# Kernel tuning notes

Hardware: AMD Instinct MI355X
Metric: run time of the kernel (lower is better)

Reference implementation:

```python
import jax, jax.numpy as jnp
import numpy as np

N = 100000   # nodes per batched graph
E = 1000000  # edges per batched graph
G = 64       # graphs in batch
D = 64       # node feature dim
H = 128      # hidden dim
L = 3        # num GCN layers
EPS = 1e-5


def setup_inputs() -> dict:
    key = jax.random.key(0)
    ks = jax.random.split(key, 20)
    def xavier(k, shape):
        fan_in, fan_out = shape[0], shape[1]
        lim = np.sqrt(6.0 / (fan_in + fan_out)).astype(np.float32)
        return jax.random.uniform(k, shape, jnp.float32, -lim, lim)
    return {
        'kernel_x': jax.random.normal(ks[0], (N, D), jnp.float32),
        'kernel_edge_index': jax.random.randint(ks[1], (2, E), 0, N, jnp.int32),
        'kernel_batch': jnp.sort(jax.random.randint(ks[2], (N,), 0, G, jnp.int32)),
        'design_x': jax.random.normal(ks[3], (N, D), jnp.float32),
        'design_edge_index': jax.random.randint(ks[4], (2, E), 0, N, jnp.int32),
        'design_batch': jnp.sort(jax.random.randint(ks[5], (N,), 0, G, jnp.int32)),
        'pragma_count': 4,
        'enc_W': xavier(ks[6], (D, H)), 'enc_b': jnp.zeros((H,), jnp.float32),
        'conv_W': jnp.stack([xavier(ks[7 + i], (H, H)) for i in range(L)]),
        'conv_b': jnp.zeros((L, H), jnp.float32),
        'ln_w': jnp.ones((L, H), jnp.float32), 'ln_b': jnp.zeros((L, H), jnp.float32),
        'head_W1': xavier(ks[10], (2 * H, H)), 'head_b1': jnp.zeros((H,), jnp.float32),
        'head_W2': xavier(ks[11], (H, H // 2)), 'head_b2': jnp.zeros((H // 2,), jnp.float32),
        'head_W3': xavier(ks[12], (H // 2, 1)), 'head_b3': jnp.zeros((1,), jnp.float32),
    }


def _gcn(x, W, b, src, dst):
    # PyG GCNConv: x' = D^{-1/2} (A + I) D^{-1/2} (x W) + b
    n = x.shape[0]
    xw = x @ W
    loop = jnp.arange(n, dtype=src.dtype)
    s = jnp.concatenate([src, loop])
    d = jnp.concatenate([dst, loop])
    deg = jax.ops.segment_sum(jnp.ones_like(d, dtype=x.dtype), d, num_segments=n)
    dinv = jax.lax.rsqrt(deg)  # deg >= 1 due to self-loops
    norm = dinv[s] * dinv[d]                       # [E+N]
    msgs = xw[s] * norm[:, None]                   # gather-transform
    return jax.ops.segment_sum(msgs, d, num_segments=n) + b


def _graph_layernorm(x, w, b, batch, num_graphs):
    # PyG LayerNorm mode='graph': normalize over all nodes+channels per graph
    n, c = x.shape
    cnt = jax.ops.segment_sum(jnp.ones((n,), x.dtype), batch, num_segments=num_graphs) * c
    mean = jax.ops.segment_sum(x.sum(axis=1), batch, num_segments=num_graphs) / cnt
    xc = x - mean[batch][:, None]
    var = jax.ops.segment_sum((xc * xc).sum(axis=1), batch, num_segments=num_graphs) / cnt
    out = xc * jax.lax.rsqrt(var + EPS)[batch][:, None]
    return out * w + b


def _encode_graph(x, edge_index, batch, enc_W, enc_b, conv_W, conv_b, ln_w, ln_b):
    src, dst = edge_index[0], edge_index[1]
    h = x @ enc_W + enc_b
    for i in range(L):
        h = _gcn(h, conv_W[i], conv_b[i], src, dst)
        h = _graph_layernorm(h, ln_w[i], ln_b[i], batch, G)
        if i < L - 1:
            h = jax.nn.relu(h)
    return jax.ops.segment_sum(h, batch, num_segments=G)  # global_add_pool -> [G, H]


def reference(kernel_x, kernel_edge_index, kernel_batch,
              design_x, design_edge_index, design_batch, pragma_count,
              enc_W, enc_b, conv_W, conv_b, ln_w, ln_b,
              head_W1, head_b1, head_W2, head_b2, head_W3, head_b3):
    design_repr = _encode_graph(design_x, design_edge_index, design_batch,
                                enc_W, enc_b, conv_W, conv_b, ln_w, ln_b)
    kernel_repr = _encode_graph(kernel_x, kernel_edge_index, kernel_batch,
                                enc_W, enc_b, conv_W, conv_b, ln_w, ln_b)
    combined = jnp.concatenate([kernel_repr, design_repr], axis=-1)  # [G, 2H]
    h = jax.nn.relu(combined @ head_W1 + head_b1)  # dropout is identity at eval
    h = jax.nn.relu(h @ head_W2 + head_b2)
    return h @ head_W3 + head_b3  # delta_pred [G, 1]
```

## Files before the change

### kernel.cpp

```cpp
#include <hip/hip_runtime.h>


#define TPB 256
#define FILL_CHUNK 2048

typedef __attribute__((ext_vector_type(8))) short bf16x8;
typedef __attribute__((ext_vector_type(8))) unsigned short u16x8;
typedef __attribute__((ext_vector_type(4))) float f32x4;
typedef __attribute__((ext_vector_type(2))) float f32x2;

__device__ __forceinline__ float bf2f(unsigned short s) {
  unsigned int u = ((unsigned int)s) << 16;
  float f;
  __builtin_memcpy(&f, &u, 4);
  return f;
}

__device__ __forceinline__ unsigned short f2bf(float f) {
  unsigned int u;
  __builtin_memcpy(&u, &f, 4);
  u = (u + 0x7FFF + ((u >> 16) & 1)) >> 16;
  return (unsigned short)u;
}

__device__ __forceinline__ void pk_acc(f32x2& acc, unsigned u) {
  union { unsigned q[2]; f32x2 f; } t;
  t.q[0] = u << 16;
  t.q[1] = u & 0xffff0000u;
  asm("v_pk_add_f32 %0, %0, %1" : "+v"(acc) : "v"(t.f));
}


__global__ __launch_bounds__(TPB) void count_dst_k(const int* __restrict__ kei,
                                                   const int* __restrict__ dei,
                                                   int* __restrict__ cnt, int E) {
  int e = blockIdx.x * TPB + threadIdx.x;
  if (e >= 2 * E) return;
  int d = (e < E) ? kei[E + e] : dei[e] + 100000;
  atomicAdd(&cnt[d], 1);
}

__global__ __launch_bounds__(TPB) void prep_node_k(const int* __restrict__ cnt,
                                                   float* __restrict__ dinv,
                                                   const int* __restrict__ kb,
                                                   const int* __restrict__ db,
                                                   int* __restrict__ batchU,
                                                   int* __restrict__ gstart,
                                                   int N, int NT) {
  int i = blockIdx.x * TPB + threadIdx.x;
  if (i >= NT) return;
  dinv[i] = 1.0f / sqrtf((float)cnt[i] + 1.0f);
  int b = (i < N) ? kb[i] : db[i - N] + 64;
  batchU[i] = b;
  if (i == 0) {
    for (int g = 0; g <= b; ++g) gstart[g] = 0;
  } else {
    int pb = (i - 1 < N) ? kb[i - 1] : db[i - 1 - N] + 64;
    for (int g = pb + 1; g <= b; ++g) gstart[g] = i;
  }
  if (i == NT - 1) {
    for (int g = b + 1; g <= 128; ++g) gstart[g] = NT;
  }
}


__global__ __launch_bounds__(TPB) void scan_partial_k(const int* __restrict__ cnt,
                                                      int* __restrict__ bsum, int n) {
  __shared__ int sd[TPB];
  int t = threadIdx.x, i0 = blockIdx.x * 512 + t * 2;
  int s = 0;
  if (i0 < n) s += cnt[i0];
  if (i0 + 1 < n) s += cnt[i0 + 1];
  sd[t] = s;
  __syncthreads();
  for (int st = TPB / 2; st > 0; st >>= 1) {
    if (t < st) sd[t] += sd[t + st];
    __syncthreads();
  }
  if (t == 0) bsum[blockIdx.x] = sd[0];
}

__global__ __launch_bounds__(512) void scan_small_k(const int* __restrict__ bsum,
                                                    int* __restrict__ bpre, int P,
                                                    int* __restrict__ rowptr, int n) {
  __shared__ int sd[512];
  int t = threadIdx.x;
  int v = (t < P) ? bsum[t] : 0;
  sd[t] = v;
  __syncthreads();
  for (int d = 1; d < 512; d <<= 1) {
    int w = (t >= d) ? sd[t - d] : 0;
    __syncthreads();
    sd[t] += w;
    __syncthreads();
  }
  if (t < P) bpre[t] = sd[t] - v;
  if (t == 511) rowptr[n] = sd[511];
}

__global__ __launch_bounds__(TPB) void scan_fill_k(const int* __restrict__ cnt,
                                                   const int* __restrict__ bpre,
                                                   int* __restrict__ rowptr,
                                                   int* __restrict__ cursor, int n) {
  __shared__ int sd[TPB];
  int t = threadIdx.x, i0 = blockIdx.x * 512 + t * 2;
  int c0 = (i0 < n) ? cnt[i0] : 0;
  int c1 = (i0 + 1 < n) ? cnt[i0 + 1] : 0;
  int s = c0 + c1;
  sd[t] = s;
  __syncthreads();
  for (int d = 1; d < TPB; d <<= 1) {
    int w = (t >= d) ? sd[t - d] : 0;
    __syncthreads();
    sd[t] += w;
    __syncthreads();
  }
  int ex = sd[t] - s + bpre[blockIdx.x];
  if (i0 < n) { rowptr[i0] = ex; cursor[i0] = ex; }
  if (i0 + 1 < n) { rowptr[i0 + 1] = ex + c0; cursor[i0 + 1] = ex + c0; }
}


__global__ __launch_bounds__(TPB) void csrfill_k(const int* __restrict__ kei,
                                                 const int* __restrict__ dei,
                                                 int* __restrict__ cursor,
                                                 int* __restrict__ csr_src,
                                                 int E, int NT) {
  int range = blockIdx.x & 7;
  int chunk = blockIdx.x >> 3;
  int nper = (NT + 7) >> 3;
  int lo = range * nper;
  int hi = lo + nper; if (hi > NT) hi = NT;
  int base = chunk * FILL_CHUNK;
  int end = base + FILL_CHUNK; if (end > 2 * E) end = 2 * E;
  const int N = NT >> 1;
  for (int e = base + threadIdx.x; e < end; e += TPB) {
    int s, d;
    if (e < E) { s = kei[e]; d = kei[E + e]; }
    else       { s = dei[e - E] + N; d = dei[e] + N; }
    if (d >= lo && d < hi) {
      int p = atomicAdd(&cursor[d], 1);
      csr_src[p] = s;
    }
  }
}


__global__ __launch_bounds__(TPB) void wprep_k(const float* __restrict__ encW,
                                               const float* __restrict__ convW,
                                               unsigned short* __restrict__ encWt,
                                               unsigned short* __restrict__ convWt) {
  int idx = blockIdx.x * TPB + threadIdx.x;
  if (idx < 64 * 128) {
    int k = idx >> 7, c = idx & 127;
    encWt[c * 64 + k] = f2bf(encW[idx]);
  }
  idx -= 64 * 128;
  if (idx >= 0 && idx < 3 * 128 * 128) {
    int l = idx >> 14, r = idx & 16383;
    int k = r >> 7, c = r & 127;
    convWt[l * 16384 + c * 128 + k] = f2bf(convW[idx]);
  }
}


template <int K, bool BIAS, bool LNRELU, bool SCALE, bool F32IN>
__global__ __launch_bounds__(TPB) void mfma_gemm_k(
    const unsigned short* __restrict__ A, const float* __restrict__ X1,
    const float* __restrict__ X2, int nsplit,
    const unsigned short* __restrict__ Wt,
    const float* __restrict__ bias, unsigned short* __restrict__ C, int nrows,
    const int* __restrict__ batch, const float* __restrict__ meanA,
    const float* __restrict__ rsigA, const float* __restrict__ lnw,
    const float* __restrict__ lnb, const float* __restrict__ dinv) {
  __shared__ short As[128 * K];
  __shared__ short Bs[128 * K];
  const int tid = threadIdx.x;
  const int r0 = blockIdx.x << 7;
  const int lane = tid & 63;
  const int wv = tid >> 6;
  const int lr = lane & 15, lg = lane >> 4;
  constexpr int CPR = K / 8;

  for (int i = tid; i < 128 * CPR; i += TPB) {
    int rloc = i / CPR, cb = i % CPR;
    int r = r0 + rloc;
    bf16x8 v = {0, 0, 0, 0, 0, 0, 0, 0};
    if (r < nrows) {
      if (F32IN) {
        const float* Af = (r < nsplit ? X1 + (long)r * K : X2 + (long)(r - nsplit) * K) + cb * 8;
        float4 f0 = *(const float4*)Af;
        float4 f1 = *(const float4*)(Af + 4);
        v[0] = (short)f2bf(f0.x); v[1] = (short)f2bf(f0.y);
        v[2] = (short)f2bf(f0.z); v[3] = (short)f2bf(f0.w);
        v[4] = (short)f2bf(f1.x); v[5] = (short)f2bf(f1.y);
        v[6] = (short)f2bf(f1.z); v[7] = (short)f2bf(f1.w);
      } else {
        v = *(const bf16x8*)(A + (long)r * K + cb * 8);
        if (LNRELU) {
          int g = batch[r];
          float m = meanA[g], rs = rsigA[g];
          int c0 = cb * 8;
#pragma unroll
          for (int j = 0; j < 8; ++j) {
            float f = bf2f((unsigned short)v[j]);
            f = (f - m) * rs * lnw[c0 + j] + lnb[c0 + j];
            f = fmaxf(f, 0.f);
            v[j] = (short)f2bf(f);
          }
        }
      }
    }
    int sb = cb ^ (rloc & 7);
    *(bf16x8*)(&As[rloc * K + sb * 8]) = v;
  }
  for (int i = tid; i < 128 * CPR; i += TPB) {
    int rloc = i / CPR, cb = i % CPR;
    bf16x8 v = *(const bf16x8*)(Wt + (long)rloc * K + cb * 8);
    int sb = cb ^ (rloc & 7);
    *(bf16x8*)(&Bs[rloc * K + sb * 8]) = v;
  }
  __syncthreads();

  f32x4 acc[2][8];
#pragma unroll
  for (int m = 0; m < 2; ++m)
#pragma unroll
    for (int n = 0; n < 8; ++n) acc[m][n] = {0.f, 0.f, 0.f, 0.f};

  const int wrow = wv * 32;
#pragma unroll
  for (int k0 = 0; k0 < K; k0 += 32) {
    const int cbk = (k0 >> 3) + lg;
    bf16x8 a[2], b[8];
#pragma unroll
    for (int m = 0; m < 2; ++m) {
      int rr = wrow + m * 16 + lr;
      int sb = cbk ^ (rr & 7);
      a[m] = *(const bf16x8*)(&As[rr * K + sb * 8]);
    }
#pragma unroll
    for (int n = 0; n < 8; ++n) {
      int rr = n * 16 + lr;
      int sb = cbk ^ (rr & 7);
      b[n] = *(const bf16x8*)(&Bs[rr * K + sb * 8]);
    }
#pragma unroll
    for (int m = 0; m < 2; ++m)
#pragma unroll
      for (int n = 0; n < 8; ++n)
        acc[m][n] = __builtin_amdgcn_mfma_f32_16x16x32_bf16(a[m], b[n], acc[m][n], 0, 0, 0);
  }

  float bv[8];
#pragma unroll
  for (int n = 0; n < 8; ++n) bv[n] = BIAS ? bias[n * 16 + lr] : 0.f;
#pragma unroll
  for (int m = 0; m < 2; ++m) {
#pragma unroll
    for (int ri = 0; ri < 4; ++ri) {
      int r = r0 + wrow + m * 16 + lg * 4 + ri;
      if (r < nrows) {
        float dv = SCALE ? dinv[r] : 1.f;
#pragma unroll
        for (int n = 0; n < 8; ++n) {
          float v = acc[m][n][ri] + bv[n];
          if (SCALE) v *= dv;
          C[(long)r * 128 + n * 16 + lr] = f2bf(v);
        }
      }
    }
  }
}


__global__ __launch_bounds__(TPB) void aggregate_k(
    const uint4* __restrict__ xws, const int* __restrict__ rowptr,
    const int* __restrict__ csr, const float* __restrict__ dinv,
    const float* __restrict__ bias, uint4* __restrict__ outb,
    float2* __restrict__ rs2, int n) {
  int wave = threadIdx.x >> 6, lane = threadIdx.x & 63;
  int d = (blockIdx.x << 2) + wave;
  if (d >= n) return;
  const int g3 = lane >> 4, cpos = lane & 15;
  f32x2 a01 = {0.f, 0.f}, a23 = {0.f, 0.f}, a45 = {0.f, 0.f}, a67 = {0.f, 0.f};

  int p0 = rowptr[d], p1 = rowptr[d + 1];
  for (int base = p0; base < p1; base += 64) {
    int idx = base + lane;
    int sl = (idx < p1) ? csr[idx] : 0;
    int cnt = p1 - base;
    if (cnt > 64) cnt = 64;
    for (int e = 0; e < cnt; e += 8) {
      int e0 = e + g3, e1 = e + 4 + g3;
      int s0 = __shfl(sl, e0);
      int s1 = __shfl(sl, e1);
      uint4 u0 = xws[(long)s0 * 16 + cpos];
      uint4 u1 = xws[(long)s1 * 16 + cpos];
      if (e0 < cnt) {
        pk_acc(a01, u0.x);
        pk_acc(a23, u0.y);
        pk_acc(a45, u0.z);
        pk_acc(a67, u0.w);
      }
      if (e1 < cnt) {
        pk_acc(a01, u1.x);
        pk_acc(a23, u1.y);
        pk_acc(a45, u1.z);
        pk_acc(a67, u1.w);
      }
    }
  }

  float acc[8] = {a01.x, a01.y, a23.x, a23.y, a45.x, a45.y, a67.x, a67.y};
#pragma unroll
  for (int j = 0; j < 8; ++j) {
    acc[j] += __shfl_xor(acc[j], 16);
    acc[j] += __shfl_xor(acc[j], 32);
  }

  uint4 su = xws[(long)d * 16 + cpos];
  float dd = dinv[d];
  float sv[8];
  sv[0] = __uint_as_float(su.x << 16);
  sv[1] = __uint_as_float(su.x & 0xffff0000u);
  sv[2] = __uint_as_float(su.y << 16);
  sv[3] = __uint_as_float(su.y & 0xffff0000u);
  sv[4] = __uint_as_float(su.z << 16);
  sv[5] = __uint_as_float(su.z & 0xffff0000u);
  sv[6] = __uint_as_float(su.w << 16);
  sv[7] = __uint_as_float(su.w & 0xffff0000u);
  const float4* b4 = (const float4*)bias;
  float4 bb0 = b4[cpos * 2];
  float4 bb1 = b4[cpos * 2 + 1];
  float val[8];
  val[0] = (acc[0] + sv[0]) * dd + bb0.x;
  val[1] = (acc[1] + sv[1]) * dd + bb0.y;
  val[2] = (acc[2] + sv[2]) * dd + bb0.z;
  val[3] = (acc[3] + sv[3]) * dd + bb0.w;
  val[4] = (acc[4] + sv[4]) * dd + bb1.x;
  val[5] = (acc[5] + sv[5]) * dd + bb1.y;
  val[6] = (acc[6] + sv[6]) * dd + bb1.z;
  val[7] = (acc[7] + sv[7]) * dd + bb1.w;

  if (g3 == 0) {
    uint4 o;
    o.x = (unsigned)f2bf(val[0]) | ((unsigned)f2bf(val[1]) << 16);
    o.y = (unsigned)f2bf(val[2]) | ((unsigned)f2bf(val[3]) << 16);
    o.z = (unsigned)f2bf(val[4]) | ((unsigned)f2bf(val[5]) << 16);
    o.w = (unsigned)f2bf(val[6]) | ((unsigned)f2bf(val[7]) << 16);
    outb[(long)d * 16 + cpos] = o;
  }

  float s1 = 0.f, s2 = 0.f;
#pragma unroll
  for (int j = 0; j < 8; ++j) {
    s1 += val[j];
    s2 += val[j] * val[j];
  }
#pragma unroll
  for (int m = 8; m >= 1; m >>= 1) {
    s1 += __shfl_xor(s1, m);
    s2 += __shfl_xor(s2, m);
  }
  if (lane == 0) rs2[d] = make_float2(s1, s2);
}


__global__ __launch_bounds__(TPB) void gstats_k(const float2* __restrict__ rs2,
                                                const int* __restrict__ gstart,
                                                float* __restrict__ meanA,
                                                float* __restrict__ rsigA,
                                                float* __restrict__ cntA) {
  __shared__ double sd1[TPB], sd2[TPB];
  int g = blockIdx.x, t = threadIdx.x;
  int n0 = gstart[g], n1 = gstart[g + 1];
  double s1 = 0, s2 = 0;
  for (int i = n0 + t; i < n1; i += TPB) {
    float2 v = rs2[i];
    s1 += v.x; s2 += v.y;
  }
  sd1[t] = s1; sd2[t] = s2;
  __syncthreads();
  for (int st = TPB / 2; st > 0; st >>= 1) {
    if (t < st) { sd1[t] += sd1[t + st]; sd2[t] += sd2[t + st]; }
    __syncthreads();
  }
  if (t == 0) {
    double cntd = (double)(n1 - n0) * 128.0;
    if (cntd > 0.0) {
      double mean = sd1[0] / cntd;
      double var = sd2[0] / cntd - mean * mean;
      if (var < 0.0) var = 0.0;
      meanA[g] = (float)mean;
      rsigA[g] = (float)(1.0 / sqrt(var + 1e-5));
    } else {
      meanA[g] = 0.f;
      rsigA[g] = 0.f;
    }
    cntA[g] = (float)(n1 - n0);
  }
}


__global__ __launch_bounds__(TPB) void pool_k(const unsigned short* __restrict__ x,
                                              const int* __restrict__ gstart,
                                              float* __restrict__ part) {
  __shared__ float red[16][132];
  int g = blockIdx.x >> 3, s = blockIdx.x & 7;
  int tid = threadIdx.x;
  int ro = tid >> 4, c8 = tid & 15;
  int n0 = gstart[g], n1 = gstart[g + 1];
  float acc[8];
#pragma unroll
  for (int j = 0; j < 8; ++j) acc[j] = 0.f;
  for (int nn = n0 + s + ro * 8; nn < n1; nn += 8 * 16) {
    u16x8 v = *(const u16x8*)(x + (long)nn * 128 + c8 * 8);
#pragma unroll
    for (int j = 0; j < 8; ++j) acc[j] += bf2f(v[j]);
  }
#pragma unroll
  for (int j = 0; j < 8; ++j) red[ro][c8 * 8 + j] = acc[j];
  __syncthreads();
  for (int st = 8; st > 0; st >>= 1) {
    if (ro < st) {
#pragma unroll
      for (int j = 0; j < 8; ++j) red[ro][c8 * 8 + j] += red[ro + st][c8 * 8 + j];
    }
    __syncthreads();
  }
  if (tid < 128) part[((long)s * 128 + g) * 128 + tid] = red[0][tid];
}


__global__ __launch_bounds__(TPB) void head_k(
    const float* __restrict__ part, const float* __restrict__ meanU,
    const float* __restrict__ rsigU, const float* __restrict__ cntU,
    const float* __restrict__ lnw2, const float* __restrict__ lnb2,
    const float* __restrict__ W1, const float* __restrict__ b1,
    const float* __restrict__ W2, const float* __restrict__ b2,
    const float* __restrict__ W3, const float* __restrict__ b3,
    float* __restrict__ out) {
  __shared__ float ps[256];
  __shared__ float prt[256];
  __shared__ float h1[128];
  __shared__ float h2[64];
  int g = blockIdx.x, tid = threadIdx.x;
  {
    int j = tid & 127, side = tid >> 7;
    int gg = side ? 64 + g : g;
    float S = 0.f;
#pragma unroll
    for (int s = 0; s < 8; ++s) S += part[((long)s * 128 + gg) * 128 + j];
    float m = meanU[gg], r = rsigU[gg], c = cntU[gg];
    ps[tid] = lnw2[j] * r * (S - m * c) + lnb2[j] * c;
  }
  __syncthreads();
  {
    int j = tid & 127, half = tid >> 7;
    float acc = 0.f;
    const float* w = W1 + (size_t)half * 128 * 128 + j;
    const float* p = ps + half * 128;
#pragma unroll 8
    for (int k = 0; k < 128; ++k) acc = fmaf(p[k], w[(size_t)k * 128], acc);
    prt[tid] = acc;
    __syncthreads();
    if (tid < 128) h1[tid] = fmaxf(prt[tid] + prt[tid + 128] + b1[tid], 0.f);
    __syncthreads();
  }
  {
    int j = tid & 63, q = tid >> 6;
    float acc = 0.f;
    const float* w = W2 + (size_t)q * 32 * 64 + j;
    const float* p = h1 + q * 32;
#pragma unroll 8
    for (int k = 0; k < 32; ++k) acc = fmaf(p[k], w[(size_t)k * 64], acc);
    prt[tid] = acc;
    __syncthreads();
    if (tid < 64)
      h2[tid] = fmaxf(prt[tid] + prt[tid + 64] + prt[tid + 128] + prt[tid + 192] + b2[tid], 0.f);
    __syncthreads();
  }
  if (tid < 64) {
    float v = h2[tid] * W3[tid];
#pragma unroll
    for (int m = 32; m >= 1; m >>= 1) v += __shfl_xor(v, m);
    if (tid == 0) out[g] = v + b3[0];
  }
}


extern "C" void kernel_launch(void* const* d_in, const int* in_sizes, int n_in,
                              void* d_out, int out_size, void* d_ws, size_t ws_size,
                              hipStream_t stream) {
  const int N = in_sizes[2];
  const int E = in_sizes[1] / 2;
  const int NT = 2 * N, ET = 2 * E;
  const int H = 128, L = 3;
  (void)n_in; (void)ws_size; (void)out_size;

  const float* kernel_x = (const float*)d_in[0];
  const int* kernel_ei  = (const int*)d_in[1];
  const int* kernel_b   = (const int*)d_in[2];
  const float* design_x = (const float*)d_in[3];
  const int* design_ei  = (const int*)d_in[4];
  const int* design_b   = (const int*)d_in[5];
  const float* encW  = (const float*)d_in[7];
  const float* encB  = (const float*)d_in[8];
  const float* convW = (const float*)d_in[9];
  const float* convB = (const float*)d_in[10];
  const float* lnw   = (const float*)d_in[11];
  const float* lnb   = (const float*)d_in[12];
  const float* W1 = (const float*)d_in[13];
  const float* b1 = (const float*)d_in[14];
  const float* W2 = (const float*)d_in[15];
  const float* b2 = (const float*)d_in[16];
  const float* W3 = (const float*)d_in[17];
  const float* b3 = (const float*)d_in[18];
  float* out = (float*)d_out;

  char* ws = (char*)d_ws;
  size_t off = 0;
  auto alloc = [&](size_t bytes) -> void* {
    void* p = ws + off;
    off = (off + bytes + 511) & ~(size_t)511;
    return p;
  };
  unsigned short* bufA = (unsigned short*)alloc((size_t)NT * H * 2);
  unsigned short* bufX = (unsigned short*)alloc((size_t)NT * H * 2);
  float* dinv    = (float*)alloc((size_t)NT * 4);
  int* cntI      = (int*)alloc((size_t)NT * 4);
  int* rowptr    = (int*)alloc((size_t)(NT + 1) * 4);
  int* cursor    = (int*)alloc((size_t)NT * 4);
  int* csr_src   = (int*)alloc((size_t)ET * 4);
  int* batchU    = (int*)alloc((size_t)NT * 4);
  int* gstart    = (int*)alloc((size_t)129 * 4);
  float2* rs2    = (float2*)alloc((size_t)NT * 8);
  float* meanS   = (float*)alloc((size_t)128 * 4);
  float* rsigS   = (float*)alloc((size_t)128 * 4);
  float* cntS    = (float*)alloc((size_t)128 * 4);
  float* meanU   = (float*)alloc((size_t)128 * 4);
  float* rsigU   = (float*)alloc((size_t)128 * 4);
  float* cntU    = (float*)alloc((size_t)128 * 4);
  float* part    = (float*)alloc((size_t)8 * 128 * 128 * 4);
  int* bsum      = (int*)alloc(512 * 4);
  int* bpre      = (int*)alloc(512 * 4);
  unsigned short* encWt  = (unsigned short*)alloc((size_t)128 * 64 * 2);
  unsigned short* convWt = (unsigned short*)alloc((size_t)L * 128 * 128 * 2);

  const int gNT   = (NT + TPB - 1) / TPB;
  const int gET   = (ET + TPB - 1) / TPB;
  const int gGemm = (NT + 127) / 128;
  const int gAgg  = (NT + 3) / 4;
  const int P     = (NT + 511) / 512;
  const int gFill = 8 * ((ET + FILL_CHUNK - 1) / FILL_CHUNK);

  wprep_k<<<(64 * 128 + 3 * 128 * 128 + TPB - 1) / TPB, TPB, 0, stream>>>(
      encW, convW, encWt, convWt);

  hipMemsetAsync(cntI, 0, (size_t)NT * 4, stream);
  count_dst_k<<<gET, TPB, 0, stream>>>(kernel_ei, design_ei, cntI, E);
  prep_node_k<<<gNT, TPB, 0, stream>>>(cntI, dinv, kernel_b, design_b, batchU,
                                       gstart, N, NT);
  scan_partial_k<<<P, TPB, 0, stream>>>(cntI, bsum, NT);
  scan_small_k<<<1, 512, 0, stream>>>(bsum, bpre, P, rowptr, NT);
  scan_fill_k<<<P, TPB, 0, stream>>>(cntI, bpre, rowptr, cursor, NT);
  csrfill_k<<<gFill, TPB, 0, stream>>>(kernel_ei, design_ei, cursor, csr_src, E, NT);

  mfma_gemm_k<64, true, false, false, true><<<gGemm, TPB, 0, stream>>>(
      nullptr, kernel_x, design_x, N, encWt, encB, bufA, NT,
      nullptr, nullptr, nullptr, nullptr, nullptr, nullptr);

  for (int i = 0; i < L; ++i) {
    float* mS = (i == L - 1) ? meanU : meanS;
    float* rS = (i == L - 1) ? rsigU : rsigS;
    float* cS = (i == L - 1) ? cntU : cntS;
    if (i == 0)
      mfma_gemm_k<128, false, false, true, false><<<gGemm, TPB, 0, stream>>>(
          bufA, nullptr, nullptr, 0, convWt + (size_t)i * H * H, nullptr, bufX, NT,
          nullptr, nullptr, nullptr, nullptr, nullptr, dinv);
    else
      mfma_gemm_k<128, false, true, true, false><<<gGemm, TPB, 0, stream>>>(
          bufA, nullptr, nullptr, 0, convWt + (size_t)i * H * H, nullptr, bufX, NT,
          batchU, meanS, rsigS, lnw + (size_t)(i - 1) * H,
          lnb + (size_t)(i - 1) * H, dinv);
    aggregate_k<<<gAgg, TPB, 0, stream>>>((const uint4*)bufX, rowptr, csr_src,
                                          dinv, convB + (size_t)i * H,
                                          (uint4*)bufA, rs2, NT);
    gstats_k<<<128, TPB, 0, stream>>>(rs2, gstart, mS, rS, cS);
  }
  pool_k<<<128 * 8, TPB, 0, stream>>>(bufA, gstart, part);

  head_k<<<64, TPB, 0, stream>>>(part, meanU, rsigU, cntU,
                                 lnw + (size_t)(L - 1) * H, lnb + (size_t)(L - 1) * H,
                                 W1, b1, W2, b2, W3, b3, out);
}
```

Baseline: 629.2 us.

## Range-partition degree counting, unroll aggregation gathers to four, enlarge fill chunk

The degree-count kernel now has each block scan a chunk of edges and apply atomics only for destinations in one of eight node ranges. This matches the range-partitioned CSR fill and is meant to improve atomic locality in L2. The aggregation loop now issues four independent gathers per iteration instead of two, raising memory-level parallelism. FILL_CHUNK doubles, which halves the grid for both the count and fill kernels. The trade-offs are that every edge index is read eight times during counting, and the wider unroll adds register pressure.

Result: no change. 625.4 us (-0.6%).

```diff
diff --git a/kernel.cpp b/kernel.cpp
--- a/kernel.cpp
+++ b/kernel.cpp
@@ -2,7 +2,7 @@
 
 
 #define TPB 256
-#define FILL_CHUNK 2048
+#define FILL_CHUNK 4096
 
 typedef __attribute__((ext_vector_type(8))) short bf16x8;
 typedef __attribute__((ext_vector_type(8))) unsigned short u16x8;
@@ -33,11 +33,20 @@
 
 __global__ __launch_bounds__(TPB) void count_dst_k(const int* __restrict__ kei,
                                                    const int* __restrict__ dei,
-                                                   int* __restrict__ cnt, int E) {
-  int e = blockIdx.x * TPB + threadIdx.x;
-  if (e >= 2 * E) return;
-  int d = (e < E) ? kei[E + e] : dei[e] + 100000;
-  atomicAdd(&cnt[d], 1);
+                                                   int* __restrict__ cnt,
+                                                   int E, int NT) {
+  int range = blockIdx.x & 7;
+  int chunk = blockIdx.x >> 3;
+  int nper = (NT + 7) >> 3;
+  int lo = range * nper;
+  int hi = lo + nper; if (hi > NT) hi = NT;
+  int base = chunk * FILL_CHUNK;
+  int end = base + FILL_CHUNK; if (end > 2 * E) end = 2 * E;
+  const int N = NT >> 1;
+  for (int e = base + threadIdx.x; e < end; e += TPB) {
+    int d = (e < E) ? kei[E + e] : dei[e] + N;
+    if (d >= lo && d < hi) atomicAdd(&cnt[d], 1);
+  }
 }
 
 __global__ __launch_bounds__(TPB) void prep_node_k(const int* __restrict__ cnt,
@@ -285,32 +294,37 @@
   const int g3 = lane >> 4, cpos = lane & 15;
   f32x2 a01 = {0.f, 0.f}, a23 = {0.f, 0.f}, a45 = {0.f, 0.f}, a67 = {0.f, 0.f};
 
+#define ACCQ(U)      \
+  {                  \
+    pk_acc(a01, (U).x); \
+    pk_acc(a23, (U).y); \
+    pk_acc(a45, (U).z); \
+    pk_acc(a67, (U).w); \
+  }
+
   int p0 = rowptr[d], p1 = rowptr[d + 1];
   for (int base = p0; base < p1; base += 64) {
     int idx = base + lane;
     int sl = (idx < p1) ? csr[idx] : 0;
     int cnt = p1 - base;
     if (cnt > 64) cnt = 64;
-    for (int e = 0; e < cnt; e += 8) {
-      int e0 = e + g3, e1 = e + 4 + g3;
+    for (int e = 0; e < cnt; e += 16) {
+      int e0 = e + g3, e1 = e + 4 + g3, e2 = e + 8 + g3, e3 = e + 12 + g3;
       int s0 = __shfl(sl, e0);
       int s1 = __shfl(sl, e1);
+      int s2 = __shfl(sl, e2);
+      int s3 = __shfl(sl, e3);
       uint4 u0 = xws[(long)s0 * 16 + cpos];
       uint4 u1 = xws[(long)s1 * 16 + cpos];
-      if (e0 < cnt) {
-        pk_acc(a01, u0.x);
-        pk_acc(a23, u0.y);
-        pk_acc(a45, u0.z);
-        pk_acc(a67, u0.w);
-      }
-      if (e1 < cnt) {
-        pk_acc(a01, u1.x);
-        pk_acc(a23, u1.y);
-        pk_acc(a45, u1.z);
-        pk_acc(a67, u1.w);
-      }
-    }
-  }
+      uint4 u2 = xws[(long)s2 * 16 + cpos];
+      uint4 u3 = xws[(long)s3 * 16 + cpos];
+      if (e0 < cnt) ACCQ(u0);
+      if (e1 < cnt) ACCQ(u1);
+      if (e2 < cnt) ACCQ(u2);
+      if (e3 < cnt) ACCQ(u3);
+    }
+  }
+#undef ACCQ
 
   float acc[8] = {a01.x, a01.y, a23.x, a23.y, a45.x, a45.y, a67.x, a67.y};
 #pragma unroll
@@ -549,7 +563,6 @@
   unsigned short* convWt = (unsigned short*)alloc((size_t)L * 128 * 128 * 2);
 
   const int gNT   = (NT + TPB - 1) / TPB;
-  const int gET   = (ET + TPB - 1) / TPB;
   const int gGemm = (NT + 127) / 128;
   const int gAgg  = (NT + 3) / 4;
   const int P     = (NT + 511) / 512;
@@ -559,7 +572,7 @@
       encW, convW, encWt, convWt);
 
   hipMemsetAsync(cntI, 0, (size_t)NT * 4, stream);
-  count_dst_k<<<gET, TPB, 0, stream>>>(kernel_ei, design_ei, cntI, E);
+  count_dst_k<<<gFill, TPB, 0, stream>>>(kernel_ei, design_ei, cntI, E, NT);
   prep_node_k<<<gNT, TPB, 0, stream>>>(cntI, dinv, kernel_b, design_b, batchU,
                                        gstart, N, NT);
   scan_partial_k<<<P, TPB, 0, stream>>>(cntI, bsum, NT);
```
